# Performance work log

Measured on AMD Instinct MI355X. Metric: run time of the kernel, lower is better.

The kernel has to match this reference:

```python
import jax, jax.numpy as jnp
import numpy as np

GAMMA = 10.0   # RBF width of the stand-in radial kernel
EPS = 1e-12    # safe-norm epsilon (avoids NaN grad at zero difference)

N_POINTS = 16384
N_NBR = 32
C_IN = 16
C_OUT = 16
N_BASIS = 16


def setup_inputs() -> dict:
    key = jax.random.key(0)
    k1, k2, k3, k4, k5, k6 = jax.random.split(key, 6)
    inp = jax.random.normal(k1, (C_IN, N_POINTS), dtype=jnp.float32)
    coords = jax.random.normal(k2, (N_POINTS, 3), dtype=jnp.float32)
    W = jax.random.normal(k3, (C_OUT, C_IN, N_BASIS), dtype=jnp.float32)
    centers = jax.random.uniform(k4, (N_BASIS,), dtype=jnp.float32)
    relative_mask = jax.random.uniform(k5, (N_POINTS, N_NBR), dtype=jnp.float32)
    neighbors = jax.random.randint(k6, (N_POINTS, N_NBR), 0, N_POINTS)
    return {"input": inp, "coords": coords, "W": W, "centers": centers,
            "relative_mask": relative_mask, "neighbors": neighbors}


def reference(input, coords, W, centers, relative_mask, neighbors):
    # difference_matrix: [N, K, 3]
    diff = coords[neighbors] - coords[:, None, :]
    # edge length with safe sqrt: [N, K]
    r = jnp.sqrt(jnp.sum(diff * diff, axis=-1) + EPS)
    # Gaussian radial basis: [N, K, B]
    rbf = jnp.exp(-GAMMA * (r[..., None] - centers) ** 2)
    # per-edge kernel: [C_out, C_in, N, K]
    kernel = jnp.einsum('oib,nkb->oink', W, rbf)
    # relative_mask applied as einsum 'ba,dcba->dcba'
    kernel = relative_mask * kernel
    # neighbor feature gather: [C_in, N, K]
    neighbors_input = input[:, neighbors]
    # contraction 'cba,dcba->db': [C_out, N]
    output = jnp.einsum('ink,oink->on', neighbors_input, kernel)
    return output
```

## Files before the change

### kernel.cpp

```cpp
#include <hip/hip_runtime.h>
#include <hip/hip_bf16.h>

#define NPTS 16384
#define NNBR 32
#define CIN 16
#define COUT 16
#define NBASIS 16

#define WF_OS 264
#define ML_PS 264

typedef _Float16 half8 __attribute__((ext_vector_type(8)));
typedef float floatx4 __attribute__((ext_vector_type(4)));

#define WS_XT 0
#define WS_C4 (NPTS * CIN)
#define WS_WF (WS_C4 + NPTS * 4 * 2)

__global__ __launch_bounds__(256) void prep_kernel(
        const float* __restrict__ input, const float* __restrict__ coords,
        const float* __restrict__ W, _Float16* __restrict__ ws) {
    const int n = blockIdx.x * 256 + threadIdx.x;
    _Float16 v[CIN];
    #pragma unroll
    for (int i = 0; i < CIN; ++i) v[i] = (_Float16)input[i * NPTS + n];
    *(half8*)&ws[WS_XT + n * CIN]     = *(half8*)&v[0];
    *(half8*)&ws[WS_XT + n * CIN + 8] = *(half8*)&v[8];
    float4* c4 = (float4*)&ws[WS_C4];
    c4[n] = make_float4(coords[n * 3 + 0], coords[n * 3 + 1], coords[n * 3 + 2], 0.0f);
    if (blockIdx.x == 0) {
        const int o = threadIdx.x >> 4, b = threadIdx.x & 15;
        _Float16 w[16];
        #pragma unroll
        for (int i = 0; i < CIN; ++i) w[i] = (_Float16)W[o * 256 + i * 16 + b];
        *(half8*)&ws[WS_WF + o * 256 + b * 16]     = *(half8*)&w[0];
        *(half8*)&ws[WS_WF + o * 256 + b * 16 + 8] = *(half8*)&w[8];
    }
}

__global__ __launch_bounds__(256) void se3_conv_kernel(
        const _Float16* __restrict__ ws,
        const float* __restrict__ centers,
        const float* __restrict__ mask,
        const int* __restrict__ neighbors,
        float* __restrict__ out) {
    __shared__ _Float16 Wf[COUT * WF_OS];
    __shared__ _Float16 Mld[16 * ML_PS];

    const int tid = threadIdx.x;
    const int t = tid & 15;
    const int quad = (tid >> 4) & 3;
    const int wv = tid >> 6;
    const int nbase = blockIdx.x * 16;

    const _Float16* xT16 = &ws[WS_XT];
    const float4* coords4 = (const float4*)&ws[WS_C4];

    {
        const int o = tid >> 4, ch = tid & 15;
        const half8 w0 = *(const half8*)&ws[WS_WF + o * 256 + ch * 16];
        const half8 w1 = *(const half8*)&ws[WS_WF + o * 256 + ch * 16 + 8];
        *(half8*)&Wf[o * WF_OS + ch * 16]     = w0;
        *(half8*)&Wf[o * WF_OS + ch * 16 + 8] = w1;
    }

    const float cb = centers[t];
    #pragma unroll
    for (int q = 0; q < 4; ++q) {
        const int pq = wv * 4 + q;
        const int n = nbase + pq;
        const int kb = n * NNBR + 8 * quad;
        const int4 n0 = *(const int4*)&neighbors[kb];
        const int4 n1 = *(const int4*)&neighbors[kb + 4];
        const float4 m0 = *(const float4*)&mask[kb];
        const float4 m1 = *(const float4*)&mask[kb + 4];
        const float4 cc = coords4[n];
        const int nb[8] = {n0.x & (NPTS - 1), n0.y & (NPTS - 1),
                           n0.z & (NPTS - 1), n0.w & (NPTS - 1),
                           n1.x & (NPTS - 1), n1.y & (NPTS - 1),
                           n1.z & (NPTS - 1), n1.w & (NPTS - 1)};
        const float mj[8] = {m0.x, m0.y, m0.z, m0.w, m1.x, m1.y, m1.z, m1.w};
        half8 af, bf;
        #pragma unroll
        for (int j = 0; j < 8; ++j) {
            const float4 cj = coords4[nb[j]];
            const float dx = cj.x - cc.x, dy = cj.y - cc.y, dz = cj.z - cc.z;
            const float r = sqrtf(dx * dx + dy * dy + dz * dz + 1e-12f);
            const float d = r - cb;
            bf[j] = (_Float16)__expf(-10.0f * d * d);
            const float x = (float)xT16[nb[j] * CIN + t];
            af[j] = (_Float16)(x * mj[j]);
        }
        floatx4 c = {0.0f, 0.0f, 0.0f, 0.0f};
        c = __builtin_amdgcn_mfma_f32_16x16x32_f16(af, bf, c, 0, 0, 0);
        _Float16 h[4];
        #pragma unroll
        for (int v = 0; v < 4; ++v) h[v] = (_Float16)c[v];
        *(uint2*)&Mld[pq * ML_PS + t * 16 + 4 * quad] = *(uint2*)h;
    }
    __syncthreads();

    floatx4 acc = {0.0f, 0.0f, 0.0f, 0.0f};
    #pragma unroll
    for (int cch = 0; cch < 8; ++cch) {
        const int bi = cch * 32 + 8 * quad;
        const half8 a = *(const half8*)&Wf[t * WF_OS + bi];
        const half8 b = *(const half8*)&Mld[t * ML_PS + bi];
        acc = __builtin_amdgcn_mfma_f32_16x16x32_f16(a, b, acc, 0, 0, 0);
    }
    if (wv == (t >> 2)) {
        #pragma unroll
        for (int v = 0; v < 4; ++v)
            out[(4 * quad + v) * NPTS + nbase + t] = acc[v];
    }
}

extern "C" void kernel_launch(void* const* d_in, const int* in_sizes, int n_in,
                              void* d_out, int out_size, void* d_ws, size_t ws_size,
                              hipStream_t stream) {
    const float* input   = (const float*)d_in[0];
    const float* coords  = (const float*)d_in[1];
    const float* W       = (const float*)d_in[2];
    const float* centers = (const float*)d_in[3];
    const float* mask    = (const float*)d_in[4];
    const int*   nbr     = (const int*)d_in[5];
    float* out = (float*)d_out;
    _Float16* ws = (_Float16*)d_ws;

    prep_kernel<<<NPTS / 256, 256, 0, stream>>>(input, coords, W, ws);
    se3_conv_kernel<<<NPTS / 16, 256, 0, stream>>>(ws, centers, mask, nbr, out);
}
```

Before: 76.89 us.

## Fuse prep into conv kernel with atomic grid barrier and interleaved point records

Removes the separate prep kernel. Each block now writes its own 16 points as fp16 features plus fp32 coordinates into one 64-byte record per point, then waits on a global atomic counter as a grid-wide barrier before the gather phase. Packing features and coordinates per point lets each neighbor gather touch one cache line instead of two arrays, and fusing avoids a second kernel launch and the weight staging through workspace. The cost is an extra memset per call and a spin barrier that assumes all 1024 blocks are resident at once (launch_bounds 256,4). It has a timeout fallback that could silently read incomplete data if they are not.

```diff
diff --git a/kernel.cpp b/kernel.cpp
--- a/kernel.cpp
+++ b/kernel.cpp
@@ -6,63 +6,66 @@
 #define CIN 16
 #define COUT 16
 #define NBASIS 16
+#define NBLK (NPTS / 16)
 
 #define WF_OS 264
 #define ML_PS 264
 
+#define CTR_BYTE_OFF (32u << 20)
+
 typedef _Float16 half8 __attribute__((ext_vector_type(8)));
 typedef float floatx4 __attribute__((ext_vector_type(4)));
 
-#define WS_XT 0
-#define WS_C4 (NPTS * CIN)
-#define WS_WF (WS_C4 + NPTS * 4 * 2)
-
-__global__ __launch_bounds__(256) void prep_kernel(
-        const float* __restrict__ input, const float* __restrict__ coords,
-        const float* __restrict__ W, _Float16* __restrict__ ws) {
-    const int n = blockIdx.x * 256 + threadIdx.x;
-    _Float16 v[CIN];
-    #pragma unroll
-    for (int i = 0; i < CIN; ++i) v[i] = (_Float16)input[i * NPTS + n];
-    *(half8*)&ws[WS_XT + n * CIN]     = *(half8*)&v[0];
-    *(half8*)&ws[WS_XT + n * CIN + 8] = *(half8*)&v[8];
-    float4* c4 = (float4*)&ws[WS_C4];
-    c4[n] = make_float4(coords[n * 3 + 0], coords[n * 3 + 1], coords[n * 3 + 2], 0.0f);
-    if (blockIdx.x == 0) {
-        const int o = threadIdx.x >> 4, b = threadIdx.x & 15;
-        _Float16 w[16];
-        #pragma unroll
-        for (int i = 0; i < CIN; ++i) w[i] = (_Float16)W[o * 256 + i * 16 + b];
-        *(half8*)&ws[WS_WF + o * 256 + b * 16]     = *(half8*)&w[0];
-        *(half8*)&ws[WS_WF + o * 256 + b * 16 + 8] = *(half8*)&w[8];
-    }
-}
-
-__global__ __launch_bounds__(256) void se3_conv_kernel(
-        const _Float16* __restrict__ ws,
+__global__ __launch_bounds__(256, 4) void se3_fused_kernel(
+        const float* __restrict__ input,
+        const float* __restrict__ coords,
+        const float* __restrict__ W,
         const float* __restrict__ centers,
         const float* __restrict__ mask,
         const int* __restrict__ neighbors,
-        float* __restrict__ out) {
+        float* __restrict__ out,
+        _Float16* __restrict__ rec16,
+        unsigned int* __restrict__ ctr) {
     __shared__ _Float16 Wf[COUT * WF_OS];
     __shared__ _Float16 Mld[16 * ML_PS];
 
     const int tid = threadIdx.x;
     const int t = tid & 15;
+    const int p = tid >> 4;
     const int quad = (tid >> 4) & 3;
     const int wv = tid >> 6;
     const int nbase = blockIdx.x * 16;
 
-    const _Float16* xT16 = &ws[WS_XT];
-    const float4* coords4 = (const float4*)&ws[WS_C4];
+    {
+        const int n = nbase + p;
+        rec16[n * 32 + t] = (_Float16)input[t * NPTS + n];
+        if (t < 3) ((float*)rec16)[n * 16 + 8 + t] = coords[n * 3 + t];
+    }
+    __syncthreads();
+    if (tid == 0) {
+        __builtin_amdgcn_fence(__ATOMIC_RELEASE, "agent");
+        __hip_atomic_fetch_add(ctr, 1u, __ATOMIC_RELAXED, __HIP_MEMORY_SCOPE_AGENT);
+    }
 
     {
-        const int o = tid >> 4, ch = tid & 15;
-        const half8 w0 = *(const half8*)&ws[WS_WF + o * 256 + ch * 16];
-        const half8 w1 = *(const half8*)&ws[WS_WF + o * 256 + ch * 16 + 8];
-        *(half8*)&Wf[o * WF_OS + ch * 16]     = w0;
-        *(half8*)&Wf[o * WF_OS + ch * 16 + 8] = w1;
+        const int o = tid >> 4, b = tid & 15;
+        _Float16 w[16];
+        #pragma unroll
+        for (int i = 0; i < CIN; ++i) w[i] = (_Float16)W[o * 256 + i * 16 + b];
+        *(half8*)&Wf[o * WF_OS + b * 16]     = *(half8*)&w[0];
+        *(half8*)&Wf[o * WF_OS + b * 16 + 8] = *(half8*)&w[8];
     }
+
+    if (tid == 0) {
+        int iters = 0;
+        while (__hip_atomic_load(ctr, __ATOMIC_RELAXED,
+                                 __HIP_MEMORY_SCOPE_AGENT) < (unsigned)NBLK) {
+            if (++iters > 100000) break;
+            __builtin_amdgcn_s_sleep(1);
+        }
+        __builtin_amdgcn_fence(__ATOMIC_ACQUIRE, "agent");
+    }
+    __syncthreads();
 
     const float cb = centers[t];
     #pragma unroll
@@ -74,7 +77,8 @@
         const int4 n1 = *(const int4*)&neighbors[kb + 4];
         const float4 m0 = *(const float4*)&mask[kb];
         const float4 m1 = *(const float4*)&mask[kb + 4];
-        const float4 cc = coords4[n];
+        const float* cc = (const float*)&rec16[n * 32 + 16];
+        const float ccx = cc[0], ccy = cc[1], ccz = cc[2];
         const int nb[8] = {n0.x & (NPTS - 1), n0.y & (NPTS - 1),
                            n0.z & (NPTS - 1), n0.w & (NPTS - 1),
                            n1.x & (NPTS - 1), n1.y & (NPTS - 1),
@@ -83,13 +87,13 @@
         half8 af, bf;
         #pragma unroll
         for (int j = 0; j < 8; ++j) {
-            const float4 cj = coords4[nb[j]];
-            const float dx = cj.x - cc.x, dy = cj.y - cc.y, dz = cj.z - cc.z;
+            const _Float16* xr = &rec16[nb[j] * 32];
+            const float* cr = (const float*)(xr + 16);
+            const float dx = cr[0] - ccx, dy = cr[1] - ccy, dz = cr[2] - ccz;
             const float r = sqrtf(dx * dx + dy * dy + dz * dz + 1e-12f);
             const float d = r - cb;
             bf[j] = (_Float16)__expf(-10.0f * d * d);
-            const float x = (float)xT16[nb[j] * CIN + t];
-            af[j] = (_Float16)(x * mj[j]);
+            af[j] = (_Float16)((float)xr[t] * mj[j]);
         }
         floatx4 c = {0.0f, 0.0f, 0.0f, 0.0f};
         c = __builtin_amdgcn_mfma_f32_16x16x32_f16(af, bf, c, 0, 0, 0);
@@ -125,8 +129,10 @@
     const float* mask    = (const float*)d_in[4];
     const int*   nbr     = (const int*)d_in[5];
     float* out = (float*)d_out;
-    _Float16* ws = (_Float16*)d_ws;
+    _Float16* rec16 = (_Float16*)d_ws;
+    unsigned int* ctr = (unsigned int*)((char*)d_ws + CTR_BYTE_OFF);
 
-    prep_kernel<<<NPTS / 256, 256, 0, stream>>>(input, coords, W, ws);
-    se3_conv_kernel<<<NPTS / 16, 256, 0, stream>>>(ws, centers, mask, nbr, out);
+    hipMemsetAsync(ctr, 0, sizeof(unsigned int), stream);
+    se3_fused_kernel<<<NBLK, 256, 0, stream>>>(input, coords, W, centers,
+                                               mask, nbr, out, rec16, ctr);
 }
```

Measured after the change: 127.7 us. +66.1%, slower.

## Precompute edge lengths in prep kernel and batch gathers in conv kernel

Applied to the files above, without the earlier changes.

Moves the per-edge distance computation (neighbor coordinate gather and sqrt) into the prep kernel, which now launches one thread per edge and writes a float radius array to workspace. The main kernel reads radii contiguously instead of gathering float4 coordinates. It also issues all neighbor, mask and radius loads for its four points up front, then all feature gathers, to raise memory-level parallelism. It adds launch_bounds min-blocks of 2. The cost is an extra 2 MB radius write and read, plus a much larger prep grid, and more live registers in the conv kernel.

```diff
diff --git a/kernel.cpp b/kernel.cpp
--- a/kernel.cpp
+++ b/kernel.cpp
@@ -13,33 +13,43 @@
 typedef _Float16 half8 __attribute__((ext_vector_type(8)));
 typedef float floatx4 __attribute__((ext_vector_type(4)));
 
-#define WS_XT 0
-#define WS_C4 (NPTS * CIN)
-#define WS_WF (WS_C4 + NPTS * 4 * 2)
+#define WS_XT_OFF 0
+#define WS_WF_OFF (512 * 1024)
+#define WS_RR_OFF (1024 * 1024)
 
 __global__ __launch_bounds__(256) void prep_kernel(
         const float* __restrict__ input, const float* __restrict__ coords,
-        const float* __restrict__ W, _Float16* __restrict__ ws) {
-    const int n = blockIdx.x * 256 + threadIdx.x;
-    _Float16 v[CIN];
-    #pragma unroll
-    for (int i = 0; i < CIN; ++i) v[i] = (_Float16)input[i * NPTS + n];
-    *(half8*)&ws[WS_XT + n * CIN]     = *(half8*)&v[0];
-    *(half8*)&ws[WS_XT + n * CIN + 8] = *(half8*)&v[8];
-    float4* c4 = (float4*)&ws[WS_C4];
-    c4[n] = make_float4(coords[n * 3 + 0], coords[n * 3 + 1], coords[n * 3 + 2], 0.0f);
-    if (blockIdx.x == 0) {
+        const float* __restrict__ W, const int* __restrict__ neighbors,
+        char* __restrict__ ws) {
+    const int f = blockIdx.x * 256 + threadIdx.x;
+    const int n = f >> 5;
+    const int nbr = neighbors[f] & (NPTS - 1);
+    const float dx = coords[nbr * 3 + 0] - coords[n * 3 + 0];
+    const float dy = coords[nbr * 3 + 1] - coords[n * 3 + 1];
+    const float dz = coords[nbr * 3 + 2] - coords[n * 3 + 2];
+    ((float*)(ws + WS_RR_OFF))[f] = sqrtf(dx * dx + dy * dy + dz * dz + 1e-12f);
+
+    if (blockIdx.x < NPTS / 256) {
+        const int n2 = blockIdx.x * 256 + threadIdx.x;
+        _Float16 v[CIN];
+        #pragma unroll
+        for (int i = 0; i < CIN; ++i) v[i] = (_Float16)input[i * NPTS + n2];
+        _Float16* xT16 = (_Float16*)(ws + WS_XT_OFF);
+        *(half8*)&xT16[n2 * CIN]     = *(half8*)&v[0];
+        *(half8*)&xT16[n2 * CIN + 8] = *(half8*)&v[8];
+    } else if (blockIdx.x == NPTS / 256) {
         const int o = threadIdx.x >> 4, b = threadIdx.x & 15;
         _Float16 w[16];
         #pragma unroll
         for (int i = 0; i < CIN; ++i) w[i] = (_Float16)W[o * 256 + i * 16 + b];
-        *(half8*)&ws[WS_WF + o * 256 + b * 16]     = *(half8*)&w[0];
-        *(half8*)&ws[WS_WF + o * 256 + b * 16 + 8] = *(half8*)&w[8];
+        _Float16* wf = (_Float16*)(ws + WS_WF_OFF);
+        *(half8*)&wf[o * 256 + b * 16]     = *(half8*)&w[0];
+        *(half8*)&wf[o * 256 + b * 16 + 8] = *(half8*)&w[8];
     }
 }
 
-__global__ __launch_bounds__(256) void se3_conv_kernel(
-        const _Float16* __restrict__ ws,
+__global__ __launch_bounds__(256, 2) void se3_conv_kernel(
+        const char* __restrict__ ws,
         const float* __restrict__ centers,
         const float* __restrict__ mask,
         const int* __restrict__ neighbors,
@@ -47,52 +57,66 @@
     __shared__ _Float16 Wf[COUT * WF_OS];
     __shared__ _Float16 Mld[16 * ML_PS];
 
+    const _Float16* xT16 = (const _Float16*)(ws + WS_XT_OFF);
+    const float* rr = (const float*)(ws + WS_RR_OFF);
+
     const int tid = threadIdx.x;
     const int t = tid & 15;
     const int quad = (tid >> 4) & 3;
     const int wv = tid >> 6;
     const int nbase = blockIdx.x * 16;
 
-    const _Float16* xT16 = &ws[WS_XT];
-    const float4* coords4 = (const float4*)&ws[WS_C4];
-
     {
         const int o = tid >> 4, ch = tid & 15;
-        const half8 w0 = *(const half8*)&ws[WS_WF + o * 256 + ch * 16];
-        const half8 w1 = *(const half8*)&ws[WS_WF + o * 256 + ch * 16 + 8];
+        const _Float16* wf = (const _Float16*)(ws + WS_WF_OFF);
+        const half8 w0 = *(const half8*)&wf[o * 256 + ch * 16];
+        const half8 w1 = *(const half8*)&wf[o * 256 + ch * 16 + 8];
         *(half8*)&Wf[o * WF_OS + ch * 16]     = w0;
         *(half8*)&Wf[o * WF_OS + ch * 16 + 8] = w1;
     }
 
     const float cb = centers[t];
+
+    int4 n0[4], n1[4];
+    float4 m0[4], m1[4], r0[4], r1[4];
     #pragma unroll
     for (int q = 0; q < 4; ++q) {
-        const int pq = wv * 4 + q;
-        const int n = nbase + pq;
-        const int kb = n * NNBR + 8 * quad;
-        const int4 n0 = *(const int4*)&neighbors[kb];
-        const int4 n1 = *(const int4*)&neighbors[kb + 4];
-        const float4 m0 = *(const float4*)&mask[kb];
-        const float4 m1 = *(const float4*)&mask[kb + 4];
-        const float4 cc = coords4[n];
-        const int nb[8] = {n0.x & (NPTS - 1), n0.y & (NPTS - 1),
-                           n0.z & (NPTS - 1), n0.w & (NPTS - 1),
-                           n1.x & (NPTS - 1), n1.y & (NPTS - 1),
-                           n1.z & (NPTS - 1), n1.w & (NPTS - 1)};
-        const float mj[8] = {m0.x, m0.y, m0.z, m0.w, m1.x, m1.y, m1.z, m1.w};
+        const int kb = (nbase + wv * 4 + q) * NNBR + 8 * quad;
+        n0[q] = *(const int4*)&neighbors[kb];
+        n1[q] = *(const int4*)&neighbors[kb + 4];
+        m0[q] = *(const float4*)&mask[kb];
+        m1[q] = *(const float4*)&mask[kb + 4];
+        r0[q] = *(const float4*)&rr[kb];
+        r1[q] = *(const float4*)&rr[kb + 4];
+    }
+
+    float xg[4][8];
+    #pragma unroll
+    for (int q = 0; q < 4; ++q) {
+        const int nb[8] = {n0[q].x & (NPTS - 1), n0[q].y & (NPTS - 1),
+                           n0[q].z & (NPTS - 1), n0[q].w & (NPTS - 1),
+                           n1[q].x & (NPTS - 1), n1[q].y & (NPTS - 1),
+                           n1[q].z & (NPTS - 1), n1[q].w & (NPTS - 1)};
+        #pragma unroll
+        for (int j = 0; j < 8; ++j) xg[q][j] = (float)xT16[nb[j] * CIN + t];
+    }
+
+    #pragma unroll
+    for (int q = 0; q < 4; ++q) {
+        const float rj[8] = {r0[q].x, r0[q].y, r0[q].z, r0[q].w,
+                             r1[q].x, r1[q].y, r1[q].z, r1[q].w};
+        const float mj[8] = {m0[q].x, m0[q].y, m0[q].z, m0[q].w,
+                             m1[q].x, m1[q].y, m1[q].z, m1[q].w};
         half8 af, bf;
         #pragma unroll
         for (int j = 0; j < 8; ++j) {
-            const float4 cj = coords4[nb[j]];
-            const float dx = cj.x - cc.x, dy = cj.y - cc.y, dz = cj.z - cc.z;
-            const float r = sqrtf(dx * dx + dy * dy + dz * dz + 1e-12f);
-            const float d = r - cb;
+            const float d = rj[j] - cb;
             bf[j] = (_Float16)__expf(-10.0f * d * d);
-            const float x = (float)xT16[nb[j] * CIN + t];
-            af[j] = (_Float16)(x * mj[j]);
+            af[j] = (_Float16)(xg[q][j] * mj[j]);
         }
         floatx4 c = {0.0f, 0.0f, 0.0f, 0.0f};
         c = __builtin_amdgcn_mfma_f32_16x16x32_f16(af, bf, c, 0, 0, 0);
+        const int pq = wv * 4 + q;
         _Float16 h[4];
         #pragma unroll
         for (int v = 0; v < 4; ++v) h[v] = (_Float16)c[v];
@@ -125,8 +149,8 @@
     const float* mask    = (const float*)d_in[4];
     const int*   nbr     = (const int*)d_in[5];
     float* out = (float*)d_out;
-    _Float16* ws = (_Float16*)d_ws;
+    char* ws = (char*)d_ws;
 
-    prep_kernel<<<NPTS / 256, 256, 0, stream>>>(input, coords, W, ws);
+    prep_kernel<<<NPTS * NNBR / 256, 256, 0, stream>>>(input, coords, W, nbr, ws);
     se3_conv_kernel<<<NPTS / 16, 256, 0, stream>>>(ws, centers, mask, nbr, out);
 }
```

Result: no change. 76.25 us (-0.8%).

## Precompute per-edge distances in shared memory and halve points per block

Applied to the files above, without the earlier changes.

Each block now first computes every edge's distance once per thread, in a 32-edges-by-8-points layout, straight from the fp32 coords. It stores the distance, the neighbor index (as ushort) and the mask (as fp16) in shared memory. Before this, each of 16 lanes recomputed the coordinate gather and sqrt for the same edge. The prep kernel no longer writes a padded float4 coords buffer. Blocks now cover 8 points instead of 16, which doubles the grid, and launch bounds request higher occupancy. The trade-offs are half-empty tiles in the second MFMA stage, an extra __syncthreads, and lower mask precision.

```diff
diff --git a/kernel.cpp b/kernel.cpp
--- a/kernel.cpp
+++ b/kernel.cpp
@@ -11,23 +11,21 @@
 #define ML_PS 264
 
 typedef _Float16 half8 __attribute__((ext_vector_type(8)));
+typedef unsigned short ushort8 __attribute__((ext_vector_type(8)));
 typedef float floatx4 __attribute__((ext_vector_type(4)));
 
 #define WS_XT 0
-#define WS_C4 (NPTS * CIN)
-#define WS_WF (WS_C4 + NPTS * 4 * 2)
+#define WS_WF (NPTS * CIN)
 
 __global__ __launch_bounds__(256) void prep_kernel(
-        const float* __restrict__ input, const float* __restrict__ coords,
-        const float* __restrict__ W, _Float16* __restrict__ ws) {
+        const float* __restrict__ input, const float* __restrict__ W,
+        _Float16* __restrict__ ws) {
     const int n = blockIdx.x * 256 + threadIdx.x;
     _Float16 v[CIN];
     #pragma unroll
     for (int i = 0; i < CIN; ++i) v[i] = (_Float16)input[i * NPTS + n];
     *(half8*)&ws[WS_XT + n * CIN]     = *(half8*)&v[0];
     *(half8*)&ws[WS_XT + n * CIN + 8] = *(half8*)&v[8];
-    float4* c4 = (float4*)&ws[WS_C4];
-    c4[n] = make_float4(coords[n * 3 + 0], coords[n * 3 + 1], coords[n * 3 + 2], 0.0f);
     if (blockIdx.x == 0) {
         const int o = threadIdx.x >> 4, b = threadIdx.x & 15;
         _Float16 w[16];
@@ -38,23 +36,26 @@
     }
 }
 
-__global__ __launch_bounds__(256) void se3_conv_kernel(
+__global__ __launch_bounds__(256, 8) void se3_conv_kernel(
         const _Float16* __restrict__ ws,
+        const float* __restrict__ coords,
         const float* __restrict__ centers,
         const float* __restrict__ mask,
         const int* __restrict__ neighbors,
         float* __restrict__ out) {
     __shared__ _Float16 Wf[COUT * WF_OS];
-    __shared__ _Float16 Mld[16 * ML_PS];
+    __shared__ _Float16 Mld[8 * ML_PS];
+    __shared__ float    rs[8 * NNBR];
+    __shared__ unsigned short nb16[8 * NNBR];
+    __shared__ _Float16 mv16[8 * NNBR];
+
+    const _Float16* xT16 = &ws[WS_XT];
 
     const int tid = threadIdx.x;
     const int t = tid & 15;
     const int quad = (tid >> 4) & 3;
     const int wv = tid >> 6;
-    const int nbase = blockIdx.x * 16;
-
-    const _Float16* xT16 = &ws[WS_XT];
-    const float4* coords4 = (const float4*)&ws[WS_C4];
+    const int nbase = blockIdx.x * 8;
 
     {
         const int o = tid >> 4, ch = tid & 15;
@@ -64,32 +65,39 @@
         *(half8*)&Wf[o * WF_OS + ch * 16 + 8] = w1;
     }
 
+    {
+        const int pt = tid >> 5;
+        const int k = tid & 31;
+        const int n = nbase + pt;
+        const int nbr = neighbors[n * NNBR + k] & (NPTS - 1);
+        const float m = mask[n * NNBR + k];
+        const float dx = coords[nbr * 3 + 0] - coords[n * 3 + 0];
+        const float dy = coords[nbr * 3 + 1] - coords[n * 3 + 1];
+        const float dz = coords[nbr * 3 + 2] - coords[n * 3 + 2];
+        rs[tid >> 0 & 255] = 0.0f;
+        rs[pt * NNBR + k] = sqrtf(dx * dx + dy * dy + dz * dz + 1e-12f);
+        nb16[pt * NNBR + k] = (unsigned short)nbr;
+        mv16[pt * NNBR + k] = (_Float16)m;
+    }
+    __syncthreads();
+
     const float cb = centers[t];
     #pragma unroll
-    for (int q = 0; q < 4; ++q) {
-        const int pq = wv * 4 + q;
-        const int n = nbase + pq;
-        const int kb = n * NNBR + 8 * quad;
-        const int4 n0 = *(const int4*)&neighbors[kb];
-        const int4 n1 = *(const int4*)&neighbors[kb + 4];
-        const float4 m0 = *(const float4*)&mask[kb];
-        const float4 m1 = *(const float4*)&mask[kb + 4];
-        const float4 cc = coords4[n];
-        const int nb[8] = {n0.x & (NPTS - 1), n0.y & (NPTS - 1),
-                           n0.z & (NPTS - 1), n0.w & (NPTS - 1),
-                           n1.x & (NPTS - 1), n1.y & (NPTS - 1),
-                           n1.z & (NPTS - 1), n1.w & (NPTS - 1)};
-        const float mj[8] = {m0.x, m0.y, m0.z, m0.w, m1.x, m1.y, m1.z, m1.w};
+    for (int q = 0; q < 2; ++q) {
+        const int pq = wv * 2 + q;
+        const int kb = pq * NNBR + 8 * quad;
+        const float4 r0 = *(const float4*)&rs[kb];
+        const float4 r1 = *(const float4*)&rs[kb + 4];
+        const ushort8 nbv = *(const ushort8*)&nb16[kb];
+        const half8 mvv = *(const half8*)&mv16[kb];
+        const float rj[8] = {r0.x, r0.y, r0.z, r0.w, r1.x, r1.y, r1.z, r1.w};
         half8 af, bf;
         #pragma unroll
         for (int j = 0; j < 8; ++j) {
-            const float4 cj = coords4[nb[j]];
-            const float dx = cj.x - cc.x, dy = cj.y - cc.y, dz = cj.z - cc.z;
-            const float r = sqrtf(dx * dx + dy * dy + dz * dz + 1e-12f);
-            const float d = r - cb;
+            const float d = rj[j] - cb;
             bf[j] = (_Float16)__expf(-10.0f * d * d);
-            const float x = (float)xT16[nb[j] * CIN + t];
-            af[j] = (_Float16)(x * mj[j]);
+            const float x = (float)xT16[(int)nbv[j] * CIN + t];
+            af[j] = (_Float16)(x * (float)mvv[j]);
         }
         floatx4 c = {0.0f, 0.0f, 0.0f, 0.0f};
         c = __builtin_amdgcn_mfma_f32_16x16x32_f16(af, bf, c, 0, 0, 0);
@@ -105,10 +113,11 @@
     for (int cch = 0; cch < 8; ++cch) {
         const int bi = cch * 32 + 8 * quad;
         const half8 a = *(const half8*)&Wf[t * WF_OS + bi];
-        const half8 b = *(const half8*)&Mld[t * ML_PS + bi];
+        half8 b = {};
+        if (t < 8) b = *(const half8*)&Mld[t * ML_PS + bi];
         acc = __builtin_amdgcn_mfma_f32_16x16x32_f16(a, b, acc, 0, 0, 0);
     }
-    if (wv == (t >> 2)) {
+    if (t < 8 && wv == (t >> 1)) {
         #pragma unroll
         for (int v = 0; v < 4; ++v)
             out[(4 * quad + v) * NPTS + nbase + t] = acc[v];
@@ -127,6 +136,7 @@
     float* out = (float*)d_out;
     _Float16* ws = (_Float16*)d_ws;
 
-    prep_kernel<<<NPTS / 256, 256, 0, stream>>>(input, coords, W, ws);
-    se3_conv_kernel<<<NPTS / 16, 256, 0, stream>>>(ws, centers, mask, nbr, out);
+    prep_kernel<<<NPTS / 256, 256, 0, stream>>>(input, W, ws);
+    se3_conv_kernel<<<NPTS / 8, 256, 0, stream>>>(ws, coords, centers, mask,
+                                                  nbr, out);
 }
```

After: 74.37 us. 1.03x faster.
